# Optimization experiments

Hardware: AMD Instinct MI355X
Metric: run time of the kernel (lower is better)

The kernel has to match this reference:

```python
import jax, jax.numpy as jnp
import numpy as np

B, S, ENC, HID = 2, 2048, 2048, 2048
HQ, HKV, D = 8, 4, 256
SOFTCAP = 50.0
SCALING = float(256) ** -0.5  # query_pre_attn_scalar ** -0.5
EPS = 1e-6
NEG = -1e9  # finite stand-in for -inf in additive masks


def _rms_norm(x, w, eps=EPS):
    # GemmaRMSNorm: fp32 compute, scale by (1 + weight)
    xf = x.astype(jnp.float32)
    n = xf * jax.lax.rsqrt(jnp.mean(xf * xf, axis=-1, keepdims=True) + eps)
    return (n * (1.0 + w.astype(jnp.float32))).astype(x.dtype)


def _rotate_half(x):
    x1, x2 = jnp.split(x, 2, axis=-1)
    return jnp.concatenate([-x2, x1], axis=-1)


def _apply_rope(q, k, cos, sin):
    # q,k: [B, H, S, D]; cos,sin: [1, S, D] -> unsqueeze head dim
    c, s = cos[:, None, :, :], sin[:, None, :, :]
    return q * c + _rotate_half(q) * s, k * c + _rotate_half(k) * s


def setup_inputs() -> dict:
    key = jax.random.key(0)
    ks = jax.random.split(key, 8)
    hidden_states = jax.random.normal(ks[0], (B, S, HID), jnp.float32)
    encoder_hidden_states = jax.random.normal(ks[1], (B, ENC, HID), jnp.float32)
    # RoPE tables (base 10000)
    pos = jnp.arange(S, dtype=jnp.float32)
    inv_freq = 1.0 / (10000.0 ** (jnp.arange(0, D, 2, dtype=jnp.float32) / D))
    freqs = pos[:, None] * inv_freq[None, :]                 # [S, D/2]
    emb = jnp.concatenate([freqs, freqs], axis=-1)           # [S, D]
    cos = jnp.cos(emb)[None]                                 # [1, S, D]
    sin = jnp.sin(emb)[None]
    # merged additive mask: causal over self part, fully visible cross part
    causal = jnp.where(jnp.arange(S)[:, None] >= jnp.arange(S)[None, :], 0.0, NEG)
    mask = jnp.concatenate([causal, jnp.zeros((S, ENC), jnp.float32)], axis=-1)
    merged_attention_mask = mask[None, None].astype(jnp.float32)  # [1,1,S,S+ENC]
    w = 0.02
    Wq = jax.random.normal(ks[2], (HQ * D, HID), jnp.float32) * w
    Wk = jax.random.normal(ks[3], (HKV * D, HID), jnp.float32) * w
    Wv = jax.random.normal(ks[4], (HKV * D, HID), jnp.float32) * w
    Wo = jax.random.normal(ks[5], (HID, HQ * D), jnp.float32) * w
    q_norm_w = jnp.zeros((D,), jnp.float32)
    k_norm_w = jnp.zeros((D,), jnp.float32)
    return dict(hidden_states=hidden_states, encoder_hidden_states=encoder_hidden_states,
                cos=cos, sin=sin, merged_attention_mask=merged_attention_mask,
                Wq=Wq, Wk=Wk, Wv=Wv, Wo=Wo, q_norm_w=q_norm_w, k_norm_w=k_norm_w)


def reference(hidden_states, encoder_hidden_states, cos, sin, merged_attention_mask,
              Wq, Wk, Wv, Wo, q_norm_w, k_norm_w):
    b, s, _ = hidden_states.shape
    enc = encoder_hidden_states.shape[1]
    n_rep = HQ // HKV
    # projections
    q = hidden_states @ Wq.T                                 # [B,S,HQ*D]
    k_self = hidden_states @ Wk.T
    v_self = hidden_states @ Wv.T
    k_cross = encoder_hidden_states @ Wk.T
    v_cross = encoder_hidden_states @ Wv.T
    q = q.reshape(b, s, HQ, D).transpose(0, 2, 1, 3)         # [B,HQ,S,D]
    k_self = k_self.reshape(b, s, HKV, D).transpose(0, 2, 1, 3)
    v_self = v_self.reshape(b, s, HKV, D).transpose(0, 2, 1, 3)
    k_cross = k_cross.reshape(b, enc, HKV, D).transpose(0, 2, 1, 3)
    v_cross = v_cross.reshape(b, enc, HKV, D).transpose(0, 2, 1, 3)
    # QK RMSNorm + RoPE (RoPE only on self q/k)
    q = _rms_norm(q, q_norm_w)
    k_self = _rms_norm(k_self, k_norm_w)
    k_cross = _rms_norm(k_cross, k_norm_w)
    q, k_self = _apply_rope(q, k_self, cos, sin)
    # merged KV + GQA repeat
    k = jnp.concatenate([k_self, k_cross], axis=2)           # [B,HKV,S+ENC,D]
    v = jnp.concatenate([v_self, v_cross], axis=2)
    k = jnp.repeat(k, n_rep, axis=1)                         # [B,HQ,S+ENC,D]
    v = jnp.repeat(v, n_rep, axis=1)
    # eager softcapped attention
    scores = jnp.einsum('bhqd,bhkd->bhqk', q, k) * SCALING
    scores = SOFTCAP * jnp.tanh(scores / SOFTCAP)
    scores = scores + merged_attention_mask
    probs = jax.nn.softmax(scores, axis=-1)
    attn = jnp.einsum('bhqk,bhkd->bhqd', probs, v)           # [B,HQ,S,D]
    attn = attn.transpose(0, 2, 1, 3).reshape(b, s, HQ * D)
    return attn @ Wo.T
```

## Files before the change

kernel.cpp:

```cpp
#include <hip/hip_runtime.h>
#include <cstdint>

typedef __attribute__((ext_vector_type(8))) short bf16x8;
typedef __attribute__((ext_vector_type(4))) float f32x4;

#define B_ 2
#define S_ 2048
#define ENC_ 2048
#define HID_ 2048
#define HQ_ 8
#define HKV_ 4
#define D_ 256
#define L_ 4096

__device__ __forceinline__ short f2bf(float f) {
  uint32_t u = __builtin_bit_cast(uint32_t, f);
  u = (u + 0x7fffu + ((u >> 16) & 1u)) >> 16;
  return (short)u;
}
__device__ __forceinline__ float bf2f(short s) {
  uint32_t u = ((uint32_t)(uint16_t)s) << 16;
  return __builtin_bit_cast(float, u);
}
__device__ __forceinline__ uint32_t cvtpk(float lo, float hi) {
  uint32_t r;
  asm("v_cvt_pk_bf16_f32 %0, %1, %2" : "=v"(r) : "v"(lo), "v"(hi));
  return r;
}

__device__ __forceinline__ void llds16(const void* g, void* s) {
  __builtin_amdgcn_global_load_lds(
      (const __attribute__((address_space(1))) void*)(__builtin_bit_cast(uintptr_t, g)),
      (__attribute__((address_space(3))) void*)(uint32_t)(__builtin_bit_cast(uintptr_t, s)),
      16, 0, 0);
}

__device__ __forceinline__ void wg_barrier() {
  asm volatile("" ::: "memory");
  __builtin_amdgcn_s_barrier();
  asm volatile("" ::: "memory");
}

__global__ __launch_bounds__(256) void cvt_f32_bf16(const float* __restrict__ in,
                                                    short* __restrict__ out, int n) {
  int i = (blockIdx.x * 256 + threadIdx.x) * 4;
  if (i >= n) return;
  float4 v = *(const float4*)(in + i);
  short4 r;
  r.x = f2bf(v.x); r.y = f2bf(v.y); r.z = f2bf(v.z); r.w = f2bf(v.w);
  *(short4*)(out + i) = r;
}

template <int BM, int WM, int BF16OUT>
__global__ __launch_bounds__(512, 2)
void gemm_ring(const short* __restrict__ A, const short* __restrict__ Bw,
               void* __restrict__ Cout, int M, int N, int K) {
  constexpr int BN = 256;
  constexpr int LA = BM * 8 / 512;
  constexpr int LB = BN * 8 / 512;
  constexpr int LTOT = LA + LB;
  __shared__ __align__(16) short As[2][BM * 64];
  __shared__ __align__(16) short Bs[2][BN * 64];
  const int t = threadIdx.x;
  const int w = t >> 6, l = t & 63;
  const int lr = l & 15, lq = l >> 4, x7 = lr & 7;

  int nbx = N >> 8;
  int bid = blockIdx.x;
  int cpx = gridDim.x >> 3;
  int wg = (bid & 7) * cpx + (bid >> 3);
  int by = wg / nbx, bx = wg - (wg / nbx) * nbx;
  const int bm = by * BM, bn = bx * BN;
  const int wm = (w & 1) * WM, wn = (w >> 1) * 64;

  uint32_t goffA[LA], soffA[LA], goffB[LB], soffB[LB];
#pragma unroll
  for (int i = 0; i < LA; i++) {
    int slot = i * 512 + t;
    int row = slot >> 3, cp = slot & 7;
    goffA[i] = (uint32_t)((bm + row) * K + ((cp ^ (row & 7)) * 8));
    soffA[i] = (uint32_t)(slot * 8);
  }
#pragma unroll
  for (int i = 0; i < LB; i++) {
    int slot = i * 512 + t;
    int row = slot >> 3, cp = slot & 7;
    goffB[i] = (uint32_t)((bn + row) * K + ((cp ^ (row & 7)) * 8));
    soffB[i] = (uint32_t)(slot * 8);
  }

  auto stage = [&](int bufi, int k0) {
#pragma unroll
    for (int i = 0; i < LA; i++) llds16(A + (size_t)goffA[i] + k0, &As[bufi][soffA[i]]);
#pragma unroll
    for (int i = 0; i < LB; i++) llds16(Bw + (size_t)goffB[i] + k0, &Bs[bufi][soffB[i]]);
  };

  f32x4 acc[WM / 16][4];
#pragma unroll
  for (int mi = 0; mi < WM / 16; mi++)
#pragma unroll
    for (int ni = 0; ni < 4; ni++) acc[mi][ni] = f32x4{0.f, 0.f, 0.f, 0.f};

  const int NT = K >> 6;
  stage(0, 0);
  for (int tt = 0; tt < NT; tt++) {
    if (tt + 1 < NT) {
      stage((tt + 1) & 1, (tt + 1) << 6);
      if (LTOT == 8)
        asm volatile("s_waitcnt vmcnt(8)" ::: "memory");
      else
        asm volatile("s_waitcnt vmcnt(6)" ::: "memory");
    } else {
      asm volatile("s_waitcnt vmcnt(0)" ::: "memory");
    }
    wg_barrier();
    const char* Ab = (const char*)&As[tt & 1][0];
    const char* Bb = (const char*)&Bs[tt & 1][0];
#pragma unroll
    for (int ks = 0; ks < 2; ks++) {
      const int cof = ((4 * ks + lq) ^ x7) * 16;
      bf16x8 bfrag[4];
#pragma unroll
      for (int ni = 0; ni < 4; ni++)
        bfrag[ni] = *(const bf16x8*)(Bb + (wn + 16 * ni + lr) * 128 + cof);
#pragma unroll
      for (int mi = 0; mi < WM / 16; mi++) {
        bf16x8 af = *(const bf16x8*)(Ab + (wm + 16 * mi + lr) * 128 + cof);
#pragma unroll
        for (int ni = 0; ni < 4; ni++)
          acc[mi][ni] = __builtin_amdgcn_mfma_f32_16x16x32_bf16(af, bfrag[ni], acc[mi][ni], 0, 0, 0);
      }
    }
    wg_barrier();
  }

#pragma unroll
  for (int mi = 0; mi < WM / 16; mi++)
#pragma unroll
    for (int ni = 0; ni < 4; ni++)
#pragma unroll
      for (int r = 0; r < 4; r++) {
        int row = bm + wm + 16 * mi + lq * 4 + r;
        int col = bn + wn + 16 * ni + lr;
        float v = acc[mi][ni][r];
        if (BF16OUT)
          ((short*)Cout)[(size_t)row * N + col] = f2bf(v);
        else
          ((float*)Cout)[(size_t)row * N + col] = v;
      }
}

__global__ __launch_bounds__(256)
void norm_rope(const short* __restrict__ src, int src_ld, int col0, int H,
               short* __restrict__ dst, int dstL, int pos_off, int do_rope, int kswz,
               const float* __restrict__ wn, const float* __restrict__ cosp,
               const float* __restrict__ sinp) {
  __shared__ float sh[256];
  __shared__ float red[4];
  int bid = blockIdx.x;
  int s = bid & (S_ - 1);
  int h = (bid >> 11) % H;
  int b = (bid >> 11) / H;
  int d = threadIdx.x;
  int w = d >> 6, l = d & 63;
  float x = bf2f(src[(size_t)(b * S_ + s) * src_ld + col0 + h * D_ + d]);
  float ss = x * x;
#pragma unroll
  for (int off = 32; off; off >>= 1) ss += __shfl_xor(ss, off, 64);
  if (l == 0) red[w] = ss;
  __syncthreads();
  float tot = red[0] + red[1] + red[2] + red[3];
  float y = x * rsqrtf(tot * (1.0f / D_) + 1e-6f) * (1.0f + wn[d]);
  float outv = y;
  if (do_rope) {
    sh[d] = y;
    __syncthreads();
    float c = cosp[s * D_ + d];
    float sn = sinp[s * D_ + d];
    outv = (d < 128) ? (y * c - sh[d + 128] * sn) : (y * c + sh[d - 128] * sn);
  }
  int dd = d;
  if (kswz) dd = (((d >> 3) ^ (s & 7)) << 3) | (d & 7);
  dst[((size_t)(b * H + h) * dstL + pos_off + s) * D_ + dd] = f2bf(outv);
}

__global__ __launch_bounds__(256)
void v_transpose(const short* __restrict__ qkv_self, const short* __restrict__ kv_cross,
                 short* __restrict__ Vt) {
  __shared__ __align__(16) short tile[64][72];
  int bid = blockIdx.x;
  int dt = bid & 3;
  int lt = (bid >> 2) & 63;
  int h = (bid >> 8) & 3;
  int b = bid >> 10;
  int t = threadIdx.x;
  int rl = t >> 2;
  int cc = (t & 3) * 16;
  int l = lt * 64 + rl;
  const short* src;
  if (lt < 32)
    src = qkv_self + (size_t)(b * S_ + l) * 4096 + 3072 + h * D_ + dt * 64 + cc;
  else
    src = kv_cross + (size_t)(b * ENC_ + (l - S_)) * 2048 + 1024 + h * D_ + dt * 64 + cc;
  *(bf16x8*)&tile[rl][cc] = *(const bf16x8*)src;
  *(bf16x8*)&tile[rl][cc + 8] = *(const bf16x8*)(src + 8);
  __syncthreads();
  int dl = t >> 2;
  int lc = (t & 3) * 16;
  bf16x8 v0, v1;
#pragma unroll
  for (int j = 0; j < 8; j++) {
    v0[j] = tile[lc + j][dl];
    v1[j] = tile[lc + 8 + j][dl];
  }
  int d = dt * 64 + dl;
  int e3 = (dl >> 1) & 3;
  int c0 = 2 * (t & 3);
  int c1 = c0 + 1;
  int p0 = (c0 & 4) | ((c0 ^ e3) & 3);
  int p1 = (c1 & 4) | ((c1 ^ e3) & 3);
  short* rowp = Vt + ((size_t)(b * HKV_ + h) * D_ + d) * (size_t)L_ + lt * 64;
  *(bf16x8*)(rowp + p0 * 8) = v0;
  *(bf16x8*)(rowp + p1 * 8) = v1;
}

__global__ __launch_bounds__(256, 2)
void flash_attn(const short* __restrict__ Q, const short* __restrict__ K,
                const short* __restrict__ Vt, short* __restrict__ part0,
                short* __restrict__ part1, short* __restrict__ part2,
                short* __restrict__ part3, float* __restrict__ lsum) {
  __shared__ __align__(16) short Ks[2][32 * 256];
  __shared__ __align__(16) short Vs[2][256 * 32];
  __shared__ __align__(16) short Ps[4][2][16 * 40];
  int t = threadIdx.x, w = t >> 6, l = t & 63;
  int lr = l & 15, lq = l >> 4, x7 = lr & 7, vx = (lr >> 1) & 3;
  int bid = blockIdx.x;
  int pair = bid >> 6;
  int p = (bid >> 4) & 3;
  int bh = bid & 15;
  int b = bh >> 3, h = bh & 7, hk = h >> 1;
  short* op = (p == 0) ? part0 : (p == 1) ? part1 : (p == 2) ? part2 : part3;

  const short* Kbase = K + (size_t)(b * HKV_ + hk) * L_ * D_;
  const short* Vbase = Vt + (size_t)(b * HKV_ + hk) * (size_t)D_ * L_;

  uint32_t kofs[8];
#pragma unroll
  for (int kf = 0; kf < 8; kf++)
    kofs[kf] = (uint32_t)(lr * 512 + (((4 * kf + lq) ^ x7) * 16));
  const uint32_t vof = (uint32_t)(lr * 64 + ((lq ^ vx) * 16));

  const short* kg_lane = Kbase + (8 * w + (l >> 5)) * 256 + (l & 31) * 8;
  const short* vg_lane = Vbase + (size_t)(64 * w + (l >> 2)) * (size_t)L_ + (l & 3) * 8;
  short* ks_lane = &Ks[0][8 * w * 256 + l * 8];
  short* vs_lane = &Vs[0][64 * w * 32 + l * 8];

  auto stage = [&](int bufi, int k0) {
    const short* kg = kg_lane + (size_t)k0 * 256;
    short* ks = ks_lane + bufi * (32 * 256);
#pragma unroll
    for (int i = 0; i < 4; i++) llds16(kg + i * 512, ks + i * 512);
    const short* vg = vg_lane + k0;
    short* vs = vs_lane + bufi * (256 * 32);
#pragma unroll
    for (int i = 0; i < 4; i++) llds16(vg + (size_t)(16 * i) * L_, vs + i * 512);
  };

  int gi = p;
  const int lenA = 2 * pair + 34;

  for (int phase = 0; phase < 2; ++phase) {
    int qt = phase ? (15 - pair) : pair;
    int q0 = qt * 128;
    int nself = 2 * qt + 2;
    int base = phase ? lenA : 0;
    int lim = base + nself + 32;
    int qg0 = q0 + 32 * w + lr;
    int qg1 = qg0 + 16;

    bf16x8 qf0[8], qf1[8];
    {
      const short* qb0 = Q + ((size_t)(b * HQ_ + h) * S_ + qg0) * D_ + lq * 8;
      const short* qb1 = qb0 + (size_t)16 * D_;
#pragma unroll
      for (int kf = 0; kf < 8; kf++) {
        qf0[kf] = *(const bf16x8*)(qb0 + kf * 32);
        qf1[kf] = *(const bf16x8*)(qb1 + kf * 32);
      }
    }
    f32x4 o0[16], o1[16];
#pragma unroll
    for (int i = 0; i < 16; i++) {
      o0[i] = f32x4{0.f, 0.f, 0.f, 0.f};
      o1[i] = f32x4{0.f, 0.f, 0.f, 0.f};
    }
    float lacc0 = 0.f, lacc1 = 0.f;

    int gcur = gi, u = 0, buf = 0;
    {
      int local = gcur - base;
      int j = (local < nself) ? local : (local - nself + 32);
      stage(0, j * 64);
    }

    while (true) {
      int gn = gcur, un = u + 1;
      if (un == 2) { un = 0; gn = gcur + 4; }
      bool hn = (gn < lim);
      if (hn) {
        int localn = gn - base;
        int jn = (localn < nself) ? localn : (localn - nself + 32);
        stage(buf ^ 1, jn * 64 + 32 * un);
        asm volatile("s_waitcnt vmcnt(8)" ::: "memory");
      } else {
        asm volatile("s_waitcnt vmcnt(0)" ::: "memory");
      }
      wg_barrier();

      int local = gcur - base;
      int j = (local < nself) ? local : (local - nself + 32);
      int k0 = j * 64 + 32 * u;
      bool diag = (local >= nself - 2) && (local < nself);
      const char* KsB = (const char*)&Ks[buf][0];
      const char* VsB = (const char*)&Vs[buf][0];

      f32x4 sc[2][2];
#pragma unroll
      for (int nt = 0; nt < 2; nt++) {
        sc[nt][0] = f32x4{0.f, 0.f, 0.f, 0.f};
        sc[nt][1] = f32x4{0.f, 0.f, 0.f, 0.f};
      }
      __builtin_amdgcn_s_setprio(1);
#pragma unroll
      for (int kf = 0; kf < 8; kf++) {
#pragma unroll
        for (int nt = 0; nt < 2; nt++) {
          bf16x8 a = *(const bf16x8*)(KsB + kofs[kf] + nt * 8192);
          sc[nt][0] = __builtin_amdgcn_mfma_f32_16x16x32_bf16(a, qf0[kf], sc[nt][0], 0, 0, 0);
          sc[nt][1] = __builtin_amdgcn_mfma_f32_16x16x32_bf16(a, qf1[kf], sc[nt][1], 0, 0, 0);
        }
      }
      __builtin_amdgcn_s_setprio(0);

      f32x4 pe[2][2];
#pragma unroll
      for (int nt = 0; nt < 2; nt++)
#pragma unroll
        for (int qh = 0; qh < 2; qh++)
#pragma unroll
          for (int r = 0; r < 4; r++) {
            float s = sc[nt][qh][r];
            float t2 = s * s * 1.5625e-6f;
            float hh = fmaf(t2, -0.0033730157f, 0.0083333338f);
            hh = fmaf(t2, hh, -0.020833334f);
            hh = fmaf(t2, hh, 0.0625f);
            pe[nt][qh][r] = __expf(s * hh);
          }
      if (diag) {
        int kb = k0 + 4 * lq;
#pragma unroll
        for (int nt = 0; nt < 2; nt++)
#pragma unroll
          for (int r = 0; r < 4; r++) {
            if (kb + nt * 16 + r > qg0) pe[nt][0][r] = 0.f;
            if (kb + nt * 16 + r > qg1) pe[nt][1][r] = 0.f;
          }
      }
      lacc0 += (pe[0][0][0] + pe[0][0][1]) + (pe[0][0][2] + pe[0][0][3]) +
               (pe[1][0][0] + pe[1][0][1]) + (pe[1][0][2] + pe[1][0][3]);
      lacc1 += (pe[0][1][0] + pe[0][1][1]) + (pe[0][1][2] + pe[0][1][3]) +
               (pe[1][1][0] + pe[1][1][1]) + (pe[1][1][2] + pe[1][1][3]);
#pragma unroll
      for (int nt = 0; nt < 2; nt++) {
        *(uint2*)&Ps[w][0][lr * 40 + nt * 16 + lq * 4] =
            uint2{cvtpk(pe[nt][0][0], pe[nt][0][1]), cvtpk(pe[nt][0][2], pe[nt][0][3])};
        *(uint2*)&Ps[w][1][lr * 40 + nt * 16 + lq * 4] =
            uint2{cvtpk(pe[nt][1][0], pe[nt][1][1]), cvtpk(pe[nt][1][2], pe[nt][1][3])};
      }

      bf16x8 pb0 = *(const bf16x8*)&Ps[w][0][lr * 40 + lq * 8];
      bf16x8 pb1 = *(const bf16x8*)&Ps[w][1][lr * 40 + lq * 8];
      __builtin_amdgcn_s_setprio(1);
#pragma unroll
      for (int dt = 0; dt < 16; dt++) {
        bf16x8 va = *(const bf16x8*)(VsB + vof + dt * 1024);
        o0[dt] = __builtin_amdgcn_mfma_f32_16x16x32_bf16(va, pb0, o0[dt], 0, 0, 0);
        o1[dt] = __builtin_amdgcn_mfma_f32_16x16x32_bf16(va, pb1, o1[dt], 0, 0, 0);
      }
      __builtin_amdgcn_s_setprio(0);

      wg_barrier();
      if (!hn) break;
      gcur = gn; u = un; buf ^= 1;
    }
    gi = gcur + 4;

    size_t orow0 = ((size_t)b * S_ + qg0) * (HQ_ * D_) + h * D_;
    size_t orow1 = orow0 + (size_t)16 * (HQ_ * D_);
#pragma unroll
    for (int dt = 0; dt < 16; dt++) {
      *(uint2*)(op + orow0 + dt * 16 + 4 * lq) =
          uint2{cvtpk(o0[dt][0], o0[dt][1]), cvtpk(o0[dt][2], o0[dt][3])};
      *(uint2*)(op + orow1 + dt * 16 + 4 * lq) =
          uint2{cvtpk(o1[dt][0], o1[dt][1]), cvtpk(o1[dt][2], o1[dt][3])};
    }
    float lrow0 = lacc0, lrow1 = lacc1;
    lrow0 += __shfl_xor(lrow0, 16, 64);
    lrow0 += __shfl_xor(lrow0, 32, 64);
    lrow1 += __shfl_xor(lrow1, 16, 64);
    lrow1 += __shfl_xor(lrow1, 32, 64);
    if (lq == 0) {
      size_t lb = (((size_t)p * B_ + b) * HQ_ + h) * S_;
      lsum[lb + qg0] = lrow0;
      lsum[lb + qg1] = lrow1;
    }
  }
}

__global__ __launch_bounds__(256)
void combine4(const short* __restrict__ p0, const short* __restrict__ p1,
              const short* __restrict__ p2, const short* __restrict__ p3,
              const float* __restrict__ lsum, short* __restrict__ out) {
  int tid = blockIdx.x * 256 + threadIdx.x;
  size_t flat = (size_t)tid * 4;
  int h = ((int)(flat >> 8)) & 7;
  int s = ((int)(flat >> 11)) & 2047;
  int b = (int)(flat >> 22);
  size_t sbase = ((size_t)b * HQ_ + h) * S_ + s;
  const size_t SP = (size_t)B_ * HQ_ * S_;
  float inv = 1.0f / (lsum[sbase] + lsum[SP + sbase] + lsum[2 * SP + sbase] +
                      lsum[3 * SP + sbase]);
  short4 a = *(const short4*)(p0 + flat);
  short4 c = *(const short4*)(p1 + flat);
  short4 d = *(const short4*)(p2 + flat);
  short4 e = *(const short4*)(p3 + flat);
  short4 r;
  r.x = f2bf((bf2f(a.x) + bf2f(c.x) + bf2f(d.x) + bf2f(e.x)) * inv);
  r.y = f2bf((bf2f(a.y) + bf2f(c.y) + bf2f(d.y) + bf2f(e.y)) * inv);
  r.z = f2bf((bf2f(a.z) + bf2f(c.z) + bf2f(d.z) + bf2f(e.z)) * inv);
  r.w = f2bf((bf2f(a.w) + bf2f(c.w) + bf2f(d.w) + bf2f(e.w)) * inv);
  *(short4*)(out + flat) = r;
}

extern "C" void kernel_launch(void* const* d_in, const int* in_sizes, int n_in, void* d_out,
                              int out_size, void* d_ws, size_t ws_size, hipStream_t stream) {
  (void)in_sizes; (void)n_in; (void)out_size; (void)ws_size;
  const float* hidden = (const float*)d_in[0];
  const float* encoder = (const float*)d_in[1];
  const float* cosp = (const float*)d_in[2];
  const float* sinp = (const float*)d_in[3];
  const float* Wq = (const float*)d_in[5];
  const float* Wk = (const float*)d_in[6];
  const float* Wv = (const float*)d_in[7];
  const float* Wo = (const float*)d_in[8];
  const float* qnw = (const float*)d_in[9];
  const float* knw = (const float*)d_in[10];

  short* ws = (short*)d_ws;
  short* hs_bf = ws;
  short* enc_bf = ws + 8388608;
  short* wqkv_bf = ws + 16777216;
  short* wo_bf = ws + 25165824;
  short* qkv_self = ws + 29360128;
  short* kv_cross = ws + 46137344;
  short* Kb = ws + 54525952;
  short* Vtb = ws + 62914560;
  short* attn_b = hs_bf;
  short* Qb = enc_bf;
  short* part0 = qkv_self;
  short* part1 = qkv_self + 8388608;
  short* part2 = kv_cross;
  short* part3 = wqkv_bf;
  float* lsum = (float*)d_out;

  cvt_f32_bf16<<<8192, 256, 0, stream>>>(hidden, hs_bf, 8388608);
  cvt_f32_bf16<<<8192, 256, 0, stream>>>(encoder, enc_bf, 8388608);
  cvt_f32_bf16<<<4096, 256, 0, stream>>>(Wq, wqkv_bf, 4194304);
  cvt_f32_bf16<<<2048, 256, 0, stream>>>(Wk, wqkv_bf + 4194304, 2097152);
  cvt_f32_bf16<<<2048, 256, 0, stream>>>(Wv, wqkv_bf + 6291456, 2097152);
  cvt_f32_bf16<<<4096, 256, 0, stream>>>(Wo, wo_bf, 4194304);

  gemm_ring<256, 128, 1><<<256, 512, 0, stream>>>(hs_bf, wqkv_bf, qkv_self, 4096, 4096, 2048);
  gemm_ring<128, 64, 1><<<256, 512, 0, stream>>>(enc_bf, wqkv_bf + (size_t)2048 * 2048,
                                                 kv_cross, 4096, 2048, 2048);

  norm_rope<<<32768, 256, 0, stream>>>(qkv_self, 4096, 0, 8, Qb, 2048, 0, 1, 0, qnw, cosp, sinp);
  norm_rope<<<16384, 256, 0, stream>>>(qkv_self, 4096, 2048, 4, Kb, 4096, 0, 1, 1, knw, cosp, sinp);
  norm_rope<<<16384, 256, 0, stream>>>(kv_cross, 2048, 0, 4, Kb, 4096, 2048, 0, 1, knw, cosp, sinp);

  v_transpose<<<2048, 256, 0, stream>>>(qkv_self, kv_cross, Vtb);

  flash_attn<<<512, 256, 0, stream>>>(Qb, Kb, Vtb, part0, part1, part2, part3, lsum);
  combine4<<<16384, 256, 0, stream>>>(part0, part1, part2, part3, lsum, attn_b);

  gemm_ring<128, 64, 0><<<256, 512, 0, stream>>>(attn_b, wo_bf, d_out, 4096, 2048, 2048);
}
```

Baseline: 533.0 us.

## Pipeline GEMM in quarter-tile phases and use native exp2 in attention

Replaces the double-buffered GEMM with a version that splits each K-step into four quadrant phases. Each phase issues loads for half of the A or B tile into the next buffer, reads the LDS fragments it needs, and runs its MFMA block at raised priority, so global loads, LDS reads and matrix math overlap more finely. The cost is many more workgroup barriers per K-step and more complex vmcnt accounting, which could go wrong. Separately, the softcap polynomial coefficients are pre-scaled by log2(e) so the attention kernel can call v_exp_f32 directly instead of __expf, dropping one multiply per score element.

```diff
diff --git a/kernel.cpp b/kernel.cpp
--- a/kernel.cpp
+++ b/kernel.cpp
@@ -27,6 +27,11 @@
   asm("v_cvt_pk_bf16_f32 %0, %1, %2" : "=v"(r) : "v"(lo), "v"(hi));
   return r;
 }
+__device__ __forceinline__ float exp2_fast(float x) {
+  float r;
+  asm("v_exp_f32 %0, %1" : "=v"(r) : "v"(x));
+  return r;
+}
 
 __device__ __forceinline__ void llds16(const void* g, void* s) {
   __builtin_amdgcn_global_load_lds(
@@ -51,16 +56,16 @@
   *(short4*)(out + i) = r;
 }
 
-template <int BM, int WM, int BF16OUT>
+template <int BM, int BF16OUT>
 __global__ __launch_bounds__(512, 2)
-void gemm_ring(const short* __restrict__ A, const short* __restrict__ Bw,
-               void* __restrict__ Cout, int M, int N, int K) {
-  constexpr int BN = 256;
-  constexpr int LA = BM * 8 / 512;
-  constexpr int LB = BN * 8 / 512;
-  constexpr int LTOT = LA + LB;
+void gemm8p(const short* __restrict__ A, const short* __restrict__ Bw,
+            void* __restrict__ Cout, int M, int N, int K) {
+  constexpr int MF = BM / 32;
+  constexpr int MFQ = MF / 2;
+  constexpr int LCA = BM / 128;
+  constexpr int WN = LCA + 2;
   __shared__ __align__(16) short As[2][BM * 64];
-  __shared__ __align__(16) short Bs[2][BN * 64];
+  __shared__ __align__(16) short Bs[2][256 * 64];
   const int t = threadIdx.x;
   const int w = t >> 6, l = t & 63;
   const int lr = l & 15, lq = l >> 4, x7 = lr & 7;
@@ -69,74 +74,132 @@
   int bid = blockIdx.x;
   int cpx = gridDim.x >> 3;
   int wg = (bid & 7) * cpx + (bid >> 3);
-  int by = wg / nbx, bx = wg - (wg / nbx) * nbx;
-  const int bm = by * BM, bn = bx * BN;
-  const int wm = (w & 1) * WM, wn = (w >> 1) * 64;
-
-  uint32_t goffA[LA], soffA[LA], goffB[LB], soffB[LB];
-#pragma unroll
-  for (int i = 0; i < LA; i++) {
-    int slot = i * 512 + t;
-    int row = slot >> 3, cp = slot & 7;
-    goffA[i] = (uint32_t)((bm + row) * K + ((cp ^ (row & 7)) * 8));
-    soffA[i] = (uint32_t)(slot * 8);
+  int by = wg / nbx, bx = wg - by * nbx;
+  const int bm = by * BM, bn = bx * 256;
+  const int wm = (w & 1) * (BM / 2), wn = (w >> 1) * 64;
+
+  uint32_t goffA[2][LCA], soffA[2][LCA], goffB[2][2], soffB[2][2];
+#pragma unroll
+  for (int ah = 0; ah < 2; ah++)
+#pragma unroll
+    for (int i = 0; i < LCA; i++) {
+      int slot = i * 512 + t;
+      int j = slot >> 3, cp = slot & 7;
+      int row = (j / (BM / 4)) * (BM / 2) + ah * (BM / 4) + (j % (BM / 4));
+      goffA[ah][i] = (uint32_t)((bm + row) * K + ((cp ^ (row & 7)) * 8));
+      soffA[ah][i] = (uint32_t)(row * 64 + cp * 8);
+    }
+#pragma unroll
+  for (int bh = 0; bh < 2; bh++)
+#pragma unroll
+    for (int i = 0; i < 2; i++) {
+      int slot = i * 512 + t;
+      int j = slot >> 3, cp = slot & 7;
+      int row = (j >> 5) * 64 + bh * 32 + (j & 31);
+      goffB[bh][i] = (uint32_t)((bn + row) * K + ((cp ^ (row & 7)) * 8));
+      soffB[bh][i] = (uint32_t)(row * 64 + cp * 8);
+    }
+
+  auto stageA = [&](int bufi, int k0, int ah) {
+#pragma unroll
+    for (int i = 0; i < LCA; i++)
+      llds16(A + (size_t)goffA[ah][i] + k0, &As[bufi][soffA[ah][i]]);
+  };
+  auto stageB = [&](int bufi, int k0, int bh) {
+#pragma unroll
+    for (int i = 0; i < 2; i++)
+      llds16(Bw + (size_t)goffB[bh][i] + k0, &Bs[bufi][soffB[bh][i]]);
+  };
+
+  f32x4 acc[MF][4];
+#pragma unroll
+  for (int mi = 0; mi < MF; mi++)
+#pragma unroll
+    for (int ni = 0; ni < 4; ni++) acc[mi][ni] = f32x4{0.f, 0.f, 0.f, 0.f};
+
+  const int cof0 = (lq ^ x7) * 16;
+  const int cof1 = ((4 + lq) ^ x7) * 16;
+  bf16x8 a[MFQ][2], bfr[2][2];
+
+  auto rdA = [&](const char* Ab, int mh) {
+#pragma unroll
+    for (int mi = 0; mi < MFQ; mi++) {
+      int row = wm + mh * (BM / 4) + 16 * mi + lr;
+      a[mi][0] = *(const bf16x8*)(Ab + row * 128 + cof0);
+      a[mi][1] = *(const bf16x8*)(Ab + row * 128 + cof1);
+    }
+  };
+  auto rdB = [&](const char* Bb, int nh) {
+#pragma unroll
+    for (int ni = 0; ni < 2; ni++) {
+      int row = wn + nh * 32 + 16 * ni + lr;
+      bfr[ni][0] = *(const bf16x8*)(Bb + row * 128 + cof0);
+      bfr[ni][1] = *(const bf16x8*)(Bb + row * 128 + cof1);
+    }
+  };
+  auto mfmaQ = [&](int mh, int nh) {
+    __builtin_amdgcn_s_setprio(1);
+#pragma unroll
+    for (int mi = 0; mi < MFQ; mi++)
+#pragma unroll
+      for (int ni = 0; ni < 2; ni++) {
+        f32x4 c0 = acc[mh * MFQ + mi][nh * 2 + ni];
+        c0 = __builtin_amdgcn_mfma_f32_16x16x32_bf16(a[mi][0], bfr[ni][0], c0, 0, 0, 0);
+        c0 = __builtin_amdgcn_mfma_f32_16x16x32_bf16(a[mi][1], bfr[ni][1], c0, 0, 0, 0);
+        acc[mh * MFQ + mi][nh * 2 + ni] = c0;
+      }
+    __builtin_amdgcn_s_setprio(0);
+  };
+
+  const int NT = K >> 6;
+  stageA(0, 0, 0);
+  stageB(0, 0, 0);
+  stageA(0, 0, 1);
+  stageB(0, 0, 1);
+  asm volatile("s_waitcnt vmcnt(%0)" ::"i"(WN) : "memory");
+  wg_barrier();
+
+  for (int tt = 0; tt < NT; tt++) {
+    const int c = tt & 1;
+    const char* Ab = (const char*)&As[c][0];
+    const char* Bb = (const char*)&Bs[c][0];
+    const bool hn = (tt + 1 < NT);
+    const int k1 = (tt + 1) << 6;
+    if (hn) stageA(c ^ 1, k1, 0);
+    rdA(Ab, 0);
+    rdB(Bb, 0);
+    wg_barrier();
+    mfmaQ(0, 0);
+    if (hn)
+      asm volatile("s_waitcnt vmcnt(%0)" ::"i"(WN) : "memory");
+    else
+      asm volatile("s_waitcnt vmcnt(2)" ::: "memory");
+    wg_barrier();
+    if (hn) stageB(c ^ 1, k1, 0);
+    rdA(Ab, 1);
+    wg_barrier();
+    mfmaQ(1, 0);
+    if (hn)
+      asm volatile("s_waitcnt vmcnt(%0)" ::"i"(WN) : "memory");
+    else
+      asm volatile("s_waitcnt vmcnt(0)" ::: "memory");
+    wg_barrier();
+    if (hn) stageA(c ^ 1, k1, 1);
+    rdB(Bb, 1);
+    wg_barrier();
+    mfmaQ(1, 1);
+    wg_barrier();
+    if (hn) stageB(c ^ 1, k1, 1);
+    rdA(Ab, 0);
+    wg_barrier();
+    mfmaQ(0, 1);
+    if (hn)
+      asm volatile("s_waitcnt vmcnt(%0)" ::"i"(WN) : "memory");
+    wg_barrier();
   }
-#pragma unroll
-  for (int i = 0; i < LB; i++) {
-    int slot = i * 512 + t;
-    int row = slot >> 3, cp = slot & 7;
-    goffB[i] = (uint32_t)((bn + row) * K + ((cp ^ (row & 7)) * 8));
-    soffB[i] = (uint32_t)(slot * 8);
-  }
-
-  auto stage = [&](int bufi, int k0) {
-#pragma unroll
-    for (int i = 0; i < LA; i++) llds16(A + (size_t)goffA[i] + k0, &As[bufi][soffA[i]]);
-#pragma unroll
-    for (int i = 0; i < LB; i++) llds16(Bw + (size_t)goffB[i] + k0, &Bs[bufi][soffB[i]]);
-  };
-
-  f32x4 acc[WM / 16][4];
-#pragma unroll
-  for (int mi = 0; mi < WM / 16; mi++)
-#pragma unroll
-    for (int ni = 0; ni < 4; ni++) acc[mi][ni] = f32x4{0.f, 0.f, 0.f, 0.f};
-
-  const int NT = K >> 6;
-  stage(0, 0);
-  for (int tt = 0; tt < NT; tt++) {
-    if (tt + 1 < NT) {
-      stage((tt + 1) & 1, (tt + 1) << 6);
-      if (LTOT == 8)
-        asm volatile("s_waitcnt vmcnt(8)" ::: "memory");
-      else
-        asm volatile("s_waitcnt vmcnt(6)" ::: "memory");
-    } else {
-      asm volatile("s_waitcnt vmcnt(0)" ::: "memory");
-    }
-    wg_barrier();
-    const char* Ab = (const char*)&As[tt & 1][0];
-    const char* Bb = (const char*)&Bs[tt & 1][0];
-#pragma unroll
-    for (int ks = 0; ks < 2; ks++) {
-      const int cof = ((4 * ks + lq) ^ x7) * 16;
-      bf16x8 bfrag[4];
-#pragma unroll
-      for (int ni = 0; ni < 4; ni++)
-        bfrag[ni] = *(const bf16x8*)(Bb + (wn + 16 * ni + lr) * 128 + cof);
-#pragma unroll
-      for (int mi = 0; mi < WM / 16; mi++) {
-        bf16x8 af = *(const bf16x8*)(Ab + (wm + 16 * mi + lr) * 128 + cof);
-#pragma unroll
-        for (int ni = 0; ni < 4; ni++)
-          acc[mi][ni] = __builtin_amdgcn_mfma_f32_16x16x32_bf16(af, bfrag[ni], acc[mi][ni], 0, 0, 0);
-      }
-    }
-    wg_barrier();
-  }
-
-#pragma unroll
-  for (int mi = 0; mi < WM / 16; mi++)
+
+#pragma unroll
+  for (int mi = 0; mi < MF; mi++)
 #pragma unroll
     for (int ni = 0; ni < 4; ni++)
 #pragma unroll
@@ -352,10 +415,10 @@
           for (int r = 0; r < 4; r++) {
             float s = sc[nt][qh][r];
             float t2 = s * s * 1.5625e-6f;
-            float hh = fmaf(t2, -0.0033730157f, 0.0083333338f);
-            hh = fmaf(t2, hh, -0.020833334f);
-            hh = fmaf(t2, hh, 0.0625f);
-            pe[nt][qh][r] = __expf(s * hh);
+            float hh = fmaf(t2, -0.0048662440f, 0.0120224587f);
+            hh = fmaf(t2, hh, -0.0300561468f);
+            hh = fmaf(t2, hh, 0.0901684401f);
+            pe[nt][qh][r] = exp2_fast(s * hh);
           }
       if (diag) {
         int kb = k0 + 4 * lq;
@@ -481,9 +544,9 @@
   cvt_f32_bf16<<<2048, 256, 0, stream>>>(Wv, wqkv_bf + 6291456, 2097152);
   cvt_f32_bf16<<<4096, 256, 0, stream>>>(Wo, wo_bf, 4194304);
 
-  gemm_ring<256, 128, 1><<<256, 512, 0, stream>>>(hs_bf, wqkv_bf, qkv_self, 4096, 4096, 2048);
-  gemm_ring<128, 64, 1><<<256, 512, 0, stream>>>(enc_bf, wqkv_bf + (size_t)2048 * 2048,
-                                                 kv_cross, 4096, 2048, 2048);
+  gemm8p<256, 1><<<256, 512, 0, stream>>>(hs_bf, wqkv_bf, qkv_self, 4096, 4096, 2048);
+  gemm8p<128, 1><<<256, 512, 0, stream>>>(enc_bf, wqkv_bf + (size_t)2048 * 2048,
+                                          kv_cross, 4096, 2048, 2048);
 
   norm_rope<<<32768, 256, 0, stream>>>(qkv_self, 4096, 0, 8, Qb, 2048, 0, 1, 0, qnw, cosp, sinp);
   norm_rope<<<16384, 256, 0, stream>>>(qkv_self, 4096, 2048, 4, Kb, 4096, 0, 1, 1, knw, cosp, sinp);
@@ -494,5 +557,5 @@
   flash_attn<<<512, 256, 0, stream>>>(Qb, Kb, Vtb, part0, part1, part2, part3, lsum);
   combine4<<<16384, 256, 0, stream>>>(part0, part1, part2, part3, lsum, attn_b);
 
-  gemm_ring<128, 64, 0><<<256, 512, 0, stream>>>(attn_b, wo_bf, d_out, 4096, 2048, 2048);
-}
+  gemm8p<128, 0><<<256, 512, 0, stream>>>(attn_b, wo_bf, d_out, 4096, 2048, 2048);
+}
```

New measurement: 549.1 us. +3.0%, slower.

## Restructure GEMMs to 256-thread blocks with K=32 tiles; use native exp2 in attention

Applied to the files above, without the earlier changes.

Replaces the 512-thread GEMM with a 256-thread variant that uses a K-step of 32. Each wave covers all 128 rows and a slice of the columns, and MFMA issue is wrapped in raised scheduling priority. The grid doubles to 512 blocks, and LDS use per block shrinks. Separately, the softcap/exp polynomial coefficients are pre-scaled by log2(e) so the attention kernel can call v_exp_f32 directly and drop the extra multiply inside __expf. The K=32 tile doubles the number of barriers per K and raises register pressure from the 8xNF accumulators.

```diff
diff --git a/kernel.cpp b/kernel.cpp
--- a/kernel.cpp
+++ b/kernel.cpp
@@ -27,6 +27,11 @@
   asm("v_cvt_pk_bf16_f32 %0, %1, %2" : "=v"(r) : "v"(lo), "v"(hi));
   return r;
 }
+__device__ __forceinline__ float exp2_fast(float x) {
+  float r;
+  asm("v_exp_f32 %0, %1" : "=v"(r) : "v"(x));
+  return r;
+}
 
 __device__ __forceinline__ void llds16(const void* g, void* s) {
   __builtin_amdgcn_global_load_lds(
@@ -51,97 +56,97 @@
   *(short4*)(out + i) = r;
 }
 
-template <int BM, int WM, int BF16OUT>
-__global__ __launch_bounds__(512, 2)
-void gemm_ring(const short* __restrict__ A, const short* __restrict__ Bw,
-               void* __restrict__ Cout, int M, int N, int K) {
-  constexpr int BN = 256;
-  constexpr int LA = BM * 8 / 512;
-  constexpr int LB = BN * 8 / 512;
+template <int BM, int BN, int BF16OUT>
+__global__ __launch_bounds__(256, 2)
+void gemm_ring2(const short* __restrict__ A, const short* __restrict__ Bw,
+                void* __restrict__ Cout, int M, int N, int K) {
+  constexpr int NF = BN / 64;
+  constexpr int LA = BM / 64;
+  constexpr int LB = BN / 64;
   constexpr int LTOT = LA + LB;
-  __shared__ __align__(16) short As[2][BM * 64];
-  __shared__ __align__(16) short Bs[2][BN * 64];
+  __shared__ __align__(16) short As[2][BM * 32];
+  __shared__ __align__(16) short Bs[2][BN * 32];
   const int t = threadIdx.x;
   const int w = t >> 6, l = t & 63;
-  const int lr = l & 15, lq = l >> 4, x7 = lr & 7;
-
-  int nbx = N >> 8;
+  const int lr = l & 15, lq = l >> 4;
+
+  int nbx = N / BN;
   int bid = blockIdx.x;
   int cpx = gridDim.x >> 3;
   int wg = (bid & 7) * cpx + (bid >> 3);
-  int by = wg / nbx, bx = wg - (wg / nbx) * nbx;
+  int by = wg / nbx, bx = wg - by * nbx;
   const int bm = by * BM, bn = bx * BN;
-  const int wm = (w & 1) * WM, wn = (w >> 1) * 64;
-
-  uint32_t goffA[LA], soffA[LA], goffB[LB], soffB[LB];
+  const int wn = w * (BN / 4);
+
+  uint32_t goffA[LA], goffB[LB];
 #pragma unroll
   for (int i = 0; i < LA; i++) {
-    int slot = i * 512 + t;
-    int row = slot >> 3, cp = slot & 7;
-    goffA[i] = (uint32_t)((bm + row) * K + ((cp ^ (row & 7)) * 8));
-    soffA[i] = (uint32_t)(slot * 8);
+    int slot = i * 256 + t;
+    int row = slot >> 2, cp = slot & 3;
+    goffA[i] = (uint32_t)((bm + row) * K + ((cp ^ (row & 3)) * 8));
   }
 #pragma unroll
   for (int i = 0; i < LB; i++) {
-    int slot = i * 512 + t;
-    int row = slot >> 3, cp = slot & 7;
-    goffB[i] = (uint32_t)((bn + row) * K + ((cp ^ (row & 7)) * 8));
-    soffB[i] = (uint32_t)(slot * 8);
+    int slot = i * 256 + t;
+    int row = slot >> 2, cp = slot & 3;
+    goffB[i] = (uint32_t)((bn + row) * K + ((cp ^ (row & 3)) * 8));
   }
-
   auto stage = [&](int bufi, int k0) {
 #pragma unroll
-    for (int i = 0; i < LA; i++) llds16(A + (size_t)goffA[i] + k0, &As[bufi][soffA[i]]);
-#pragma unroll
-    for (int i = 0; i < LB; i++) llds16(Bw + (size_t)goffB[i] + k0, &Bs[bufi][soffB[i]]);
+    for (int i = 0; i < LA; i++)
+      llds16(A + (size_t)goffA[i] + k0, &As[bufi][(i * 256 + t) * 8]);
+#pragma unroll
+    for (int i = 0; i < LB; i++)
+      llds16(Bw + (size_t)goffB[i] + k0, &Bs[bufi][(i * 256 + t) * 8]);
   };
 
-  f32x4 acc[WM / 16][4];
-#pragma unroll
-  for (int mi = 0; mi < WM / 16; mi++)
-#pragma unroll
-    for (int ni = 0; ni < 4; ni++) acc[mi][ni] = f32x4{0.f, 0.f, 0.f, 0.f};
-
-  const int NT = K >> 6;
+  f32x4 acc[8][NF];
+#pragma unroll
+  for (int mi = 0; mi < 8; mi++)
+#pragma unroll
+    for (int ni = 0; ni < NF; ni++) acc[mi][ni] = f32x4{0.f, 0.f, 0.f, 0.f};
+
+  const int NT = K >> 5;
   stage(0, 0);
   for (int tt = 0; tt < NT; tt++) {
     if (tt + 1 < NT) {
-      stage((tt + 1) & 1, (tt + 1) << 6);
-      if (LTOT == 8)
-        asm volatile("s_waitcnt vmcnt(8)" ::: "memory");
-      else
-        asm volatile("s_waitcnt vmcnt(6)" ::: "memory");
+      stage((tt + 1) & 1, (tt + 1) << 5);
+      asm volatile("s_waitcnt vmcnt(%0)" ::"i"(LTOT) : "memory");
     } else {
       asm volatile("s_waitcnt vmcnt(0)" ::: "memory");
     }
     wg_barrier();
     const char* Ab = (const char*)&As[tt & 1][0];
     const char* Bb = (const char*)&Bs[tt & 1][0];
-#pragma unroll
-    for (int ks = 0; ks < 2; ks++) {
-      const int cof = ((4 * ks + lq) ^ x7) * 16;
-      bf16x8 bfrag[4];
-#pragma unroll
-      for (int ni = 0; ni < 4; ni++)
-        bfrag[ni] = *(const bf16x8*)(Bb + (wn + 16 * ni + lr) * 128 + cof);
-#pragma unroll
-      for (int mi = 0; mi < WM / 16; mi++) {
-        bf16x8 af = *(const bf16x8*)(Ab + (wm + 16 * mi + lr) * 128 + cof);
-#pragma unroll
-        for (int ni = 0; ni < 4; ni++)
-          acc[mi][ni] = __builtin_amdgcn_mfma_f32_16x16x32_bf16(af, bfrag[ni], acc[mi][ni], 0, 0, 0);
-      }
-    }
+    bf16x8 bfrag[NF], afrag[8];
+#pragma unroll
+    for (int ni = 0; ni < NF; ni++) {
+      int row = wn + 16 * ni + lr;
+      bfrag[ni] = *(const bf16x8*)(Bb + row * 64 + ((lq ^ (row & 3)) * 16));
+    }
+#pragma unroll
+    for (int mi = 0; mi < 8; mi++) {
+      int row = 16 * mi + lr;
+      afrag[mi] = *(const bf16x8*)(Ab + row * 64 + ((lq ^ (row & 3)) * 16));
+    }
+    __builtin_amdgcn_s_setprio(1);
+#pragma unroll
+    for (int mi = 0; mi < 8; mi++)
+#pragma unroll
+      for (int ni = 0; ni < NF; ni++)
+        acc[mi][ni] =
+            __builtin_amdgcn_mfma_f32_16x16x32_bf16(afrag[mi], bfrag[ni], acc[mi][ni], 0, 0, 0);
+    __builtin_amdgcn_s_setprio(0);
     wg_barrier();
   }
 
 #pragma unroll
-  for (int mi = 0; mi < WM / 16; mi++)
-#pragma unroll
-    for (int ni = 0; ni < 4; ni++)
+  for (int mi = 0; mi < 8; mi++)
+#pragma unroll
+    for (int ni = 0; ni < NF; ni++)
 #pragma unroll
       for (int r = 0; r < 4; r++) {
-        int row = bm + wm + 16 * mi + lq * 4 + r;
+        int row = bm + 16 * mi + lq * 4 + r;
         int col = bn + wn + 16 * ni + lr;
         float v = acc[mi][ni][r];
         if (BF16OUT)
@@ -352,10 +357,10 @@
           for (int r = 0; r < 4; r++) {
             float s = sc[nt][qh][r];
             float t2 = s * s * 1.5625e-6f;
-            float hh = fmaf(t2, -0.0033730157f, 0.0083333338f);
-            hh = fmaf(t2, hh, -0.020833334f);
-            hh = fmaf(t2, hh, 0.0625f);
-            pe[nt][qh][r] = __expf(s * hh);
+            float hh = fmaf(t2, -0.0048662440f, 0.0120224587f);
+            hh = fmaf(t2, hh, -0.0300561468f);
+            hh = fmaf(t2, hh, 0.0901684401f);
+            pe[nt][qh][r] = exp2_fast(s * hh);
           }
       if (diag) {
         int kb = k0 + 4 * lq;
@@ -481,9 +486,9 @@
   cvt_f32_bf16<<<2048, 256, 0, stream>>>(Wv, wqkv_bf + 6291456, 2097152);
   cvt_f32_bf16<<<4096, 256, 0, stream>>>(Wo, wo_bf, 4194304);
 
-  gemm_ring<256, 128, 1><<<256, 512, 0, stream>>>(hs_bf, wqkv_bf, qkv_self, 4096, 4096, 2048);
-  gemm_ring<128, 64, 1><<<256, 512, 0, stream>>>(enc_bf, wqkv_bf + (size_t)2048 * 2048,
-                                                 kv_cross, 4096, 2048, 2048);
+  gemm_ring2<128, 256, 1><<<512, 256, 0, stream>>>(hs_bf, wqkv_bf, qkv_self, 4096, 4096, 2048);
+  gemm_ring2<128, 128, 1><<<512, 256, 0, stream>>>(enc_bf, wqkv_bf + (size_t)2048 * 2048,
+                                                   kv_cross, 4096, 2048, 2048);
 
   norm_rope<<<32768, 256, 0, stream>>>(qkv_self, 4096, 0, 8, Qb, 2048, 0, 1, 0, qnw, cosp, sinp);
   norm_rope<<<16384, 256, 0, stream>>>(qkv_self, 4096, 2048, 4, Kb, 4096, 0, 1, 1, knw, cosp, sinp);
@@ -494,5 +499,5 @@
   flash_attn<<<512, 256, 0, stream>>>(Qb, Kb, Vtb, part0, part1, part2, part3, lsum);
   combine4<<<16384, 256, 0, stream>>>(part0, part1, part2, part3, lsum, attn_b);
 
-  gemm_ring<128, 64, 0><<<256, 512, 0, stream>>>(attn_b, wo_bf, d_out, 4096, 2048, 2048);
-}
+  gemm_ring2<128, 128, 0><<<512, 256, 0, stream>>>(attn_b, wo_bf, d_out, 4096, 2048, 2048);
+}
```

Measured after the change: 544.2 us. +2.1%, slower.
